# Kernel optimization log

Measured on AMD Instinct MI355X. Metric: run time of the kernel, lower is better.

Reference implementation:

```python
import jax, jax.numpy as jnp
import numpy as np

WS, OWS, HEADS, DH = 8, 12, 4, 16
INNER = HEADS * DH
DIM = 64
RATIO = 0.5
REL = 12  # rel_size = WS + (OWS - WS)


def _conv1x1(x, W, b):
    return jnp.einsum('oc,bchw->bohw', W, x) + b[None, :, None, None]


def _lrelu(x):
    return jnp.where(x >= 0, x, 0.1 * x)


def _rel_to_abs(x):
    # x: [b, l, 2r-1] -> [b, l, r]
    b, l, m = x.shape
    r = (m + 1) // 2
    x = jnp.pad(x, ((0, 0), (0, 0), (0, 1))).reshape(b, l * (m + 1))
    x = jnp.pad(x, ((0, 0), (0, m - l))).reshape(b, l + 1, m)
    return x[:, :l, -r:]


def _relative_logits_1d(q, rel_k):
    # q: [b, h, w, d], rel_k: [2r-1, d] -> [b, h, r, w, r]
    b, h, w, _ = q.shape
    r = (rel_k.shape[0] + 1) // 2
    logits = jnp.einsum('bxyd,rd->bxyr', q, rel_k)
    logits = _rel_to_abs(logits.reshape(b * h, w, 2 * r - 1)).reshape(b, h, w, r)
    return jnp.broadcast_to(logits[:, :, None], (b, h, r, w, r))


def _rel_pos_emb(q, rel_h, rel_w):
    # q: [b, WS*WS, DH] -> [b, WS*WS, REL*REL]
    b = q.shape[0]
    q = q.reshape(b, WS, WS, DH)
    lw = _relative_logits_1d(q, rel_w)                        # [b, x, i, y, j]
    lw = lw.transpose(0, 1, 3, 2, 4).reshape(b, WS * WS, REL * REL)   # (x y),(i j)
    lh = _relative_logits_1d(q.transpose(0, 2, 1, 3), rel_h)  # [b, y, i, x, j]
    lh = lh.transpose(0, 3, 1, 4, 2).reshape(b, WS * WS, REL * REL)   # (x y),(j i)
    return lw + lh


def _windows(t, B, Hw, Ww):
    # 'b c (h p1) (w p2) -> b (h w) (p1 p2 c)'
    return t.reshape(B, INNER, Hw, WS, Ww, WS).transpose(0, 2, 4, 3, 5, 1).reshape(B, Hw * Ww, WS * WS * INNER)


def _forward(x, condition_global, Wq, bq, Wk, bk, Wv, bv, Wout, bout,
             rel_h, rel_w, pin_W, pin_b, ln_w, ln_b, sa_W, sa_b,
             m1_W, m1_b, m2_W, m2_b):
    B, C, H, W = x.shape
    Hw, Ww = H // WS, W // WS
    Nw = Hw * Ww
    keep = int(Nw * RATIO)  # deterministic num_keep_node (expected r=0.5)
    scale = DH ** -0.5

    qs = _conv1x1(x, Wq, bq)
    ks = _conv1x1(x, Wk, bk)
    vs = _conv1x1(x, Wv, bv)

    # condition_wind: stacked ij meshgrid of linspace(-1,1,WS), tiled over windows
    lin = jnp.linspace(-1.0, 1.0, WS)
    gy, gx = jnp.meshgrid(lin, lin, indexing='ij')
    wind = jnp.tile(jnp.stack([gy, gx]).astype(x.dtype)[None], (B, 1, Hw, Ww))
    cond = jnp.concatenate([vs, condition_global, wind], axis=1)  # [B, INNER+4, H, W]

    # PredictorLG
    h1 = _conv1x1(cond, pin_W, pin_b)
    u = h1.mean(1, keepdims=True)
    s = ((h1 - u) ** 2).mean(1, keepdims=True)
    h1 = ln_w[None, :, None, None] * (h1 - u) / jnp.sqrt(s + 1e-6) + ln_b[None, :, None, None]
    h1 = _lrelu(h1)
    sa = jax.lax.conv_general_dilated(h1, sa_W, (1, 1), ((1, 1), (1, 1)),
                                      dimension_numbers=('NCHW', 'OIHW', 'NCHW'))
    sa = jax.nn.sigmoid(sa + sa_b[None, :, None, None])          # [B,1,H,W]

    xm = h1.mean(1)                                               # [B,H,W]
    xm = xm.reshape(B, Hw, WS, Ww, WS).transpose(0, 1, 3, 2, 4).reshape(B, Nw, WS * WS)
    z = _lrelu(xm @ m1_W.T + m1_b)
    pred = jax.nn.softmax(z @ m2_W.T + m2_b, axis=-1)
    score = pred[:, :, 0]
    idx = jnp.argsort(-score, axis=1)
    idx1, idx2 = idx[:, :keep], idx[:, keep:]
    bar = jnp.arange(B)[:, None]

    v_easy = vs * sa

    qw = _windows(qs, B, Hw, Ww)                                  # [B, Nw, 64*INNER]

    pad = (OWS - WS) // 2
    def unfold(t):
        p = jax.lax.conv_general_dilated_patches(t, (OWS, OWS), (WS, WS),
                                                 [(pad, pad), (pad, pad)])
        # [B, INNER*OWS*OWS, Hw, Ww], channel-major (c, kh, kw) like torch unfold
        p = p.reshape(B, INNER, OWS * OWS, Nw)
        return p.transpose(0, 3, 2, 1).reshape(B, Nw, OWS * OWS * INNER)  # (j c)
    kw, vw = unfold(ks), unfold(vs)

    qk, kk, vk = qw[bar, idx1], kw[bar, idx1], vw[bar, idx1]       # gather hard windows

    def heads(t, ntok):
        return t.reshape(B * keep, ntok, HEADS, DH).transpose(0, 2, 1, 3).reshape(B * keep * HEADS, ntok, DH)
    qh = heads(qk, WS * WS) * scale
    kh = heads(kk, OWS * OWS)
    vh = heads(vk, OWS * OWS)

    attn = jnp.einsum('bqc,bkc->bqk', qh, kh) + _rel_pos_emb(qh, rel_h, rel_w)
    attn = jax.nn.softmax(attn, axis=-1)
    vo = jnp.einsum('bqk,bkc->bqc', attn, vh)                      # [B*keep*HEADS, 64, DH]

    # '(b j head) (p1 p2) c -> b j (p1 p2 head c)'
    v1 = vo.reshape(B, keep, HEADS, WS * WS, DH).transpose(0, 1, 3, 2, 4).reshape(B, keep, WS * WS * INNER)
    v2 = _windows(v_easy, B, Hw, Ww)[bar, idx2]

    out = jnp.zeros((B, Nw, WS * WS * INNER), x.dtype)
    out = out.at[bar, idx1].set(v1).at[bar, idx2].set(v2)          # batch_index_fill
    # 'b (h w) (dh dw c) -> b c (h dh) (w dw)'
    out = out.reshape(B, Hw, Ww, WS, WS, INNER).transpose(0, 5, 1, 3, 2, 4).reshape(B, INNER, H, W)
    return _conv1x1(out, Wout, bout)


def setup_inputs() -> dict:
    key = jax.random.key(0)
    k = jax.random.split(key, 16)
    B, H, W = 2, 256, 256
    cdim = INNER + 4
    rel_scale = DH ** -0.5

    def p(kk, shape, s=0.05):
        return jax.random.normal(kk, shape, jnp.float32) * s

    return {
        'x': jax.random.normal(k[0], (B, DIM, H, W), jnp.float32),
        'condition_global': jax.random.normal(k[1], (B, 2, H, W), jnp.float32),
        'Wq': p(k[2], (INNER, DIM)), 'bq': jnp.zeros((INNER,), jnp.float32),
        'Wk': p(k[3], (INNER, DIM)), 'bk': jnp.zeros((INNER,), jnp.float32),
        'Wv': p(k[4], (INNER, DIM)), 'bv': jnp.zeros((INNER,), jnp.float32),
        'Wout': p(k[5], (DIM, INNER)), 'bout': jnp.zeros((DIM,), jnp.float32),
        'rel_h': jax.random.normal(k[6], (2 * REL - 1, DH), jnp.float32) * rel_scale,
        'rel_w': jax.random.normal(k[7], (2 * REL - 1, DH), jnp.float32) * rel_scale,
        'pin_W': p(k[8], (cdim // 4, cdim)), 'pin_b': jnp.zeros((cdim // 4,), jnp.float32),
        'ln_w': jnp.ones((cdim // 4,), jnp.float32), 'ln_b': jnp.zeros((cdim // 4,), jnp.float32),
        'sa_W': p(k[9], (1, cdim // 4, 3, 3)), 'sa_b': jnp.zeros((1,), jnp.float32),
        'm1_W': p(k[10], (WS, WS * WS)), 'm1_b': jnp.zeros((WS,), jnp.float32),
        'm2_W': p(k[11], (2, WS)), 'm2_b': jnp.zeros((2,), jnp.float32),
    }


def reference(x, condition_global, Wq, bq, Wk, bk, Wv, bv, Wout, bout,
              rel_h, rel_w, pin_W, pin_b, ln_w, ln_b, sa_W, sa_b,
              m1_W, m1_b, m2_W, m2_b):
    return _forward(x, condition_global, Wq, bq, Wk, bk, Wv, bv, Wout, bout,
                    rel_h, rel_w, pin_W, pin_b, ln_w, ln_b, sa_W, sa_b,
                    m1_W, m1_b, m2_W, m2_b)
```

## Files before the change

kernel.cpp:

```cpp
#include <hip/hip_runtime.h>
#include <math.h>

#define NPIX   65536
#define NPIXT  131072
#define NW     1024
#define KEEP   512
#define PITCH  68


__global__ __launch_bounds__(256) void k_qkv(
    const float* __restrict__ x,
    const float* __restrict__ Wq, const float* __restrict__ bq,
    const float* __restrict__ Wk, const float* __restrict__ bk,
    const float* __restrict__ Wv, const float* __restrict__ bv,
    float* __restrict__ qs, float* __restrict__ ks, float* __restrict__ vs)
{
    __shared__ float xs[64][256];
    const int tid = threadIdx.x;
    const int gp  = blockIdx.x * 256 + tid;
    const int b   = gp >> 16;
    const int p   = gp & 65535;
    const int p0  = p & ~255;

    #pragma unroll
    for (int it = 0; it < 16; ++it) {
        const int i  = it * 256 + tid;
        const int c  = i >> 6;
        const int p4 = i & 63;
        const float4 v = *(const float4*)(x + ((size_t)(b * 64 + c)) * NPIX + p0 + p4 * 4);
        *(float4*)&xs[c][p4 * 4] = v;
    }
    __syncthreads();

    const float* Ws[3]   = {Wq, Wk, Wv};
    const float* bias[3] = {bq, bk, bv};
    float* outs[3] = {qs + (size_t)gp * 64, ks + (size_t)gp * 64, vs + (size_t)gp * 64};

    for (int og = 0; og < 4; ++og) {
        float acc[3][16];
        #pragma unroll
        for (int m = 0; m < 3; ++m)
            #pragma unroll
            for (int j = 0; j < 16; ++j) acc[m][j] = 0.f;

        #pragma unroll 2
        for (int c = 0; c < 64; ++c) {
            const float xv = xs[c][tid];
            #pragma unroll
            for (int m = 0; m < 3; ++m) {
                const float* W = Ws[m];
                #pragma unroll
                for (int j = 0; j < 16; ++j)
                    acc[m][j] += W[(og * 16 + j) * 64 + c] * xv;
            }
        }
        #pragma unroll
        for (int m = 0; m < 3; ++m) {
            const float* bb = bias[m];
            #pragma unroll
            for (int j4 = 0; j4 < 4; ++j4) {
                float4 v;
                v.x = acc[m][j4 * 4 + 0] + bb[og * 16 + j4 * 4 + 0];
                v.y = acc[m][j4 * 4 + 1] + bb[og * 16 + j4 * 4 + 1];
                v.z = acc[m][j4 * 4 + 2] + bb[og * 16 + j4 * 4 + 2];
                v.w = acc[m][j4 * 4 + 3] + bb[og * 16 + j4 * 4 + 3];
                *(float4*)(outs[m] + og * 16 + j4 * 4) = v;
            }
        }
    }
}

__global__ __launch_bounds__(256) void k_cond(
    const float* __restrict__ vs, const float* __restrict__ cg,
    const float* __restrict__ pinW, const float* __restrict__ pinb,
    const float* __restrict__ lnw, const float* __restrict__ lnb,
    float* __restrict__ h1, float* __restrict__ xm)
{
    const int gp = blockIdx.x * 256 + threadIdx.x;
    const int b  = gp >> 16;
    const int p  = gp & 65535;
    const int h  = p >> 8;
    const int w  = p & 255;

    float acc[17];
    #pragma unroll
    for (int oc = 0; oc < 17; ++oc) acc[oc] = pinb[oc];

    const float* vp = vs + (size_t)gp * 64;
    #pragma unroll 4
    for (int c4 = 0; c4 < 16; ++c4) {
        const float4 v4 = *(const float4*)(vp + c4 * 4);
        const float vv[4] = {v4.x, v4.y, v4.z, v4.w};
        #pragma unroll
        for (int k = 0; k < 4; ++k) {
            const int c = c4 * 4 + k;
            #pragma unroll
            for (int oc = 0; oc < 17; ++oc)
                acc[oc] += pinW[oc * 68 + c] * vv[k];
        }
    }
    const float c64 = cg[(b * 2 + 0) * NPIX + p];
    const float c65 = cg[(b * 2 + 1) * NPIX + p];
    const float c66 = -1.f + 2.f * (float)(h & 7) / 7.f;
    const float c67 = -1.f + 2.f * (float)(w & 7) / 7.f;
    #pragma unroll
    for (int oc = 0; oc < 17; ++oc)
        acc[oc] += pinW[oc * 68 + 64] * c64 + pinW[oc * 68 + 65] * c65 +
                   pinW[oc * 68 + 66] * c66 + pinW[oc * 68 + 67] * c67;

    float u = 0.f;
    #pragma unroll
    for (int oc = 0; oc < 17; ++oc) u += acc[oc];
    u *= (1.f / 17.f);
    float s = 0.f;
    #pragma unroll
    for (int oc = 0; oc < 17; ++oc) { const float d = acc[oc] - u; s += d * d; }
    s *= (1.f / 17.f);
    const float rstd = rsqrtf(s + 1e-6f);

    float xsum = 0.f;
    #pragma unroll
    for (int oc = 0; oc < 17; ++oc) {
        float hv = lnw[oc] * (acc[oc] - u) * rstd + lnb[oc];
        hv = (hv >= 0.f) ? hv : 0.1f * hv;
        h1[(b * 17 + oc) * NPIX + p] = hv;
        xsum += hv;
    }
    xm[gp] = xsum * (1.f / 17.f);
}

__global__ __launch_bounds__(256) void k_sa(
    const float* __restrict__ h1, const float* __restrict__ saW,
    const float* __restrict__ sab, float* __restrict__ sa)
{
    __shared__ float S[17 * 3 * 256];
    const int tid = threadIdx.x;
    const int b   = blockIdx.x >> 8;
    const int row = blockIdx.x & 255;

    for (int i = tid; i < 3264; i += 256) {
        const int ch  = i / 192;
        const int rem = i - ch * 192;
        const int dr  = rem >> 6;
        const int c4  = rem & 63;
        const int rr  = row + dr - 1;
        float4 v = {0.f, 0.f, 0.f, 0.f};
        if ((unsigned)rr < 256u)
            v = *(const float4*)(h1 + ((size_t)(b * 17 + ch)) * NPIX + rr * 256 + c4 * 4);
        *(float4*)&S[(ch * 3 + dr) * 256 + c4 * 4] = v;
    }
    __syncthreads();

    const int w = tid;
    float acc = sab[0];
    #pragma unroll 1
    for (int ch = 0; ch < 17; ++ch) {
        #pragma unroll
        for (int dr = 0; dr < 3; ++dr) {
            const float* Sp = &S[(ch * 3 + dr) * 256];
            const float m  = Sp[w];
            const float l  = (w > 0)   ? Sp[w - 1] : 0.f;
            const float r_ = (w < 255) ? Sp[w + 1] : 0.f;
            const float* Wp = saW + (ch * 3 + dr) * 3;
            acc += Wp[0] * l + Wp[1] * m + Wp[2] * r_;
        }
    }
    sa[b * NPIX + row * 256 + w] = 1.f / (1.f + __expf(-acc));
}

__global__ __launch_bounds__(1024) void k_score_select(
    const float* __restrict__ xm,
    const float* __restrict__ m1W, const float* __restrict__ m1b,
    const float* __restrict__ m2W, const float* __restrict__ m2b,
    int* __restrict__ flag, int* __restrict__ kept)
{
    __shared__ float sc[NW];
    const int b = blockIdx.x;
    const int t = threadIdx.x;
    const int i = t >> 5;
    const int j = t & 31;

    float z[8];
    #pragma unroll
    for (int jj = 0; jj < 8; ++jj) z[jj] = m1b[jj];

    for (int a = 0; a < 8; ++a) {
        #pragma unroll
        for (int cc = 0; cc < 8; ++cc) {
            const float xv = xm[b * NPIX + (i * 8 + a) * 256 + (j * 8 + cc)];
            const int tt = a * 8 + cc;
            #pragma unroll
            for (int jj = 0; jj < 8; ++jj)
                z[jj] += m1W[jj * 64 + tt] * xv;
        }
    }
    #pragma unroll
    for (int jj = 0; jj < 8; ++jj) z[jj] = (z[jj] >= 0.f) ? z[jj] : 0.1f * z[jj];

    float l0 = m2b[0], l1 = m2b[1];
    #pragma unroll
    for (int jj = 0; jj < 8; ++jj) { l0 += m2W[jj] * z[jj]; l1 += m2W[8 + jj] * z[jj]; }
    const float mx = fmaxf(l0, l1);
    const float e0 = expf(l0 - mx), e1 = expf(l1 - mx);
    sc[t] = e0 / (e0 + e1);
    __syncthreads();

    const float s = sc[t];
    int cnt = 0;
    for (int jq = 0; jq < NW; ++jq) {
        const float sj = sc[jq];
        cnt += (sj > s) || (sj == s && jq < t);
    }
    flag[b * NW + t] = (cnt < KEEP) ? 1 : 0;
    if (cnt < KEEP) kept[b * KEEP + cnt] = t;
}

__global__ __launch_bounds__(256, 4) void k_attn(
    const float* __restrict__ qs, const float* __restrict__ ks,
    const float* __restrict__ vs, const int* __restrict__ kept,
    const float* __restrict__ relh, const float* __restrict__ relw,
    float* __restrict__ amix)
{
    __shared__ float SK[72 * PITCH];
    __shared__ float SV[72 * PITCH];

    const int b    = blockIdx.y;
    const int win  = kept[b * KEEP + blockIdx.x];
    const int wy = win >> 5, wx = win & 31;
    const int tid  = threadIdx.x;
    const int head = tid >> 6;
    const int lane = tid & 63;
    const int choff = head * 16;
    const size_t bbase = (size_t)b * NPIX;
    const int px0 = (wy * 8) * 256 + wx * 8;

    #pragma unroll
    for (int it = 0; it < 4; ++it) {
        const int i  = it * 256 + tid;
        const int px = i >> 4;
        const int c4 = i & 15;
        const float4 v = *(const float4*)(
            qs + (bbase + px0 + (px >> 3) * 256 + (px & 7)) * 64 + c4 * 4);
        *(float4*)&SK[px * PITCH + c4 * 4] = v;
    }
    __syncthreads();

    const int qrow = lane >> 3, qcol = lane & 7;
    float q[16];
    #pragma unroll
    for (int j4 = 0; j4 < 4; ++j4) {
        const float4 v = *(const float4*)&SK[(qrow * 8 + qcol) * PITCH + choff + j4 * 4];
        q[j4 * 4 + 0] = v.x * 0.25f; q[j4 * 4 + 1] = v.y * 0.25f;
        q[j4 * 4 + 2] = v.z * 0.25f; q[j4 * 4 + 3] = v.w * 0.25f;
    }

    float cw[12], chh[12];
    #pragma unroll
    for (int k = 0; k < 12; ++k) {
        const float* rw = relw + (k - qcol + 11) * 16;
        const float* rh = relh + (k - qrow + 11) * 16;
        float sw = 0.f, sh = 0.f;
        #pragma unroll
        for (int j4 = 0; j4 < 4; ++j4) {
            const float4 w4 = *(const float4*)(rw + j4 * 4);
            const float4 h4 = *(const float4*)(rh + j4 * 4);
            sw += q[j4*4+0]*w4.x + q[j4*4+1]*w4.y + q[j4*4+2]*w4.z + q[j4*4+3]*w4.w;
            sh += q[j4*4+0]*h4.x + q[j4*4+1]*h4.y + q[j4*4+2]*h4.z + q[j4*4+3]*h4.w;
        }
        cw[k] = sw; chh[k] = sh;
    }

    const int sub = lane >> 4;
    const int d_  = lane & 15;
    const int wy8 = wy * 8 - 2, wx8 = wx * 8 - 2;

    float sum = 0.f;
    float vo[16];
    #pragma unroll
    for (int d = 0; d < 16; ++d) vo[d] = 0.f;

    #pragma unroll 1
    for (int c = 0; c < 2; ++c) {
        __syncthreads();
        for (int i = tid; i < 1152; i += 256) {
            const int pxl = i >> 4;
            const int c4  = i & 15;
            const int rl  = pxl / 12;
            const int col = pxl - rl * 12;
            const int ry  = wy8 + 6 * c + rl;
            const int cx  = wx8 + col;
            float4 kv = {0.f,0.f,0.f,0.f}, vv = {0.f,0.f,0.f,0.f};
            if ((unsigned)ry < 256u && (unsigned)cx < 256u) {
                const size_t g = (bbase + ry * 256 + cx) * 64 + c4 * 4;
                kv = *(const float4*)(ks + g);
                vv = *(const float4*)(vs + g);
            }
            *(float4*)&SK[pxl * PITCH + c4 * 4] = kv;
            *(float4*)&SV[pxl * PITCH + c4 * 4] = vv;
        }
        __syncthreads();

        float kreg[18], vreg[18];
        #pragma unroll
        for (int r = 0; r < 18; ++r) {
            const int a = (4 * r + sub) * PITCH + choff + d_;
            kreg[r] = SK[a];
            vreg[r] = SV[a];
        }

        #pragma unroll
        for (int rl = 0; rl < 6; ++rl) {
            const float srow = chh[c * 6 + rl];
            #pragma unroll
            for (int col = 0; col < 12; ++col) {
                const int kl = rl * 12 + col;
                const int r  = kl >> 2, kk = kl & 3;
                float s = srow + cw[col];
                #pragma unroll
                for (int d = 0; d < 16; ++d)
                    s += __int_as_float(__builtin_amdgcn_readlane(
                             __float_as_int(kreg[r]), kk * 16 + d)) * q[d];
                const float e = __expf(s);
                sum += e;
                #pragma unroll
                for (int d = 0; d < 16; ++d)
                    vo[d] += e * __int_as_float(__builtin_amdgcn_readlane(
                                 __float_as_int(vreg[r]), kk * 16 + d));
            }
        }
    }

    const float inv = 1.f / sum;
    __syncthreads();
    #pragma unroll
    for (int j4 = 0; j4 < 4; ++j4) {
        float4 v;
        v.x = vo[j4*4+0] * inv; v.y = vo[j4*4+1] * inv;
        v.z = vo[j4*4+2] * inv; v.w = vo[j4*4+3] * inv;
        *(float4*)&SK[(qrow * 8 + qcol) * PITCH + choff + j4 * 4] = v;
    }
    __syncthreads();
    #pragma unroll
    for (int it = 0; it < 4; ++it) {
        const int i  = it * 256 + tid;
        const int px = i >> 4;
        const int c4 = i & 15;
        const float4 v = *(const float4*)&SK[px * PITCH + c4 * 4];
        *(float4*)(amix + (bbase + px0 + (px >> 3) * 256 + (px & 7)) * 64 + c4 * 4) = v;
    }
}

__global__ __launch_bounds__(256) void k_out_f(
    const float* __restrict__ amix, const float* __restrict__ vs,
    const float* __restrict__ sa, const int* __restrict__ flag,
    const float* __restrict__ W, const float* __restrict__ bias,
    float* __restrict__ out)
{
    __shared__ float xs[64][256];
    const int tid = threadIdx.x;
    const int gp  = blockIdx.x * 256 + tid;
    const int b   = gp >> 16;
    const int p   = gp & 65535;
    const int h   = p >> 8;
    const int w   = p & 255;

    const int win = (h >> 3) * 32 + (w >> 3);
    const int fl  = flag[b * NW + win];
    const float mult = fl ? 1.f : sa[gp];
    const float* src = (fl ? amix : vs) + (size_t)gp * 64;

    #pragma unroll
    for (int c4 = 0; c4 < 16; ++c4) {
        const float4 v = *(const float4*)(src + c4 * 4);
        xs[c4 * 4 + 0][tid] = v.x * mult;
        xs[c4 * 4 + 1][tid] = v.y * mult;
        xs[c4 * 4 + 2][tid] = v.z * mult;
        xs[c4 * 4 + 3][tid] = v.w * mult;
    }
    __syncthreads();

    const int base = (b << 6) * NPIX + p;
    for (int og = 0; og < 4; ++og) {
        float acc[16];
        #pragma unroll
        for (int j = 0; j < 16; ++j) acc[j] = 0.f;
        #pragma unroll 4
        for (int c = 0; c < 64; ++c) {
            const float xv = xs[c][tid];
            #pragma unroll
            for (int j = 0; j < 16; ++j)
                acc[j] += W[(og * 16 + j) * 64 + c] * xv;
        }
        #pragma unroll
        for (int j = 0; j < 16; ++j)
            out[base + (og * 16 + j) * NPIX] = acc[j] + bias[og * 16 + j];
    }
}

extern "C" void kernel_launch(void* const* d_in, const int* in_sizes, int n_in,
                              void* d_out, int out_size, void* d_ws, size_t ws_size,
                              hipStream_t stream)
{
    const float* x    = (const float*)d_in[0];
    const float* cg   = (const float*)d_in[1];
    const float* Wq   = (const float*)d_in[2];
    const float* bq   = (const float*)d_in[3];
    const float* Wk   = (const float*)d_in[4];
    const float* bk   = (const float*)d_in[5];
    const float* Wv   = (const float*)d_in[6];
    const float* bv   = (const float*)d_in[7];
    const float* Wout = (const float*)d_in[8];
    const float* bout = (const float*)d_in[9];
    const float* relh = (const float*)d_in[10];
    const float* relw = (const float*)d_in[11];
    const float* pinW = (const float*)d_in[12];
    const float* pinb = (const float*)d_in[13];
    const float* lnw  = (const float*)d_in[14];
    const float* lnb  = (const float*)d_in[15];
    const float* saW  = (const float*)d_in[16];
    const float* sab  = (const float*)d_in[17];
    const float* m1W  = (const float*)d_in[18];
    const float* m1b  = (const float*)d_in[19];
    const float* m2W  = (const float*)d_in[20];
    const float* m2b  = (const float*)d_in[21];
    float* out = (float*)d_out;

    float* ws    = (float*)d_ws;
    float* qs    = ws;
    float* ks    = qs + 8388608;
    float* vs    = ks + 8388608;
    float* h1    = vs + 8388608;
    float* xm    = h1 + 17 * NPIXT;
    float* sa    = xm + NPIXT;
    int*   flag  = (int*)(sa + NPIXT);
    int*   kept  = flag + 2048;

    k_qkv         <<<NPIXT / 256, 256, 0, stream>>>(x, Wq, bq, Wk, bk, Wv, bv, qs, ks, vs);
    k_cond        <<<NPIXT / 256, 256, 0, stream>>>(vs, cg, pinW, pinb, lnw, lnb, h1, xm);
    k_sa          <<<512, 256, 0, stream>>>(h1, saW, sab, sa);
    k_score_select<<<2, 1024, 0, stream>>>(xm, m1W, m1b, m2W, m2b, flag, kept);
    k_attn        <<<dim3(KEEP, 2), 256, 0, stream>>>(qs, ks, vs, kept, relh, relw, qs);
    k_out_f       <<<NPIXT / 256, 256, 0, stream>>>(qs, vs, sa, flag, Wout, bout, out);
}
```

Measured before the change: 423.4 us.

## Restructure QKV projection loop and tune waves-per-EU for qkv and attention

The QKV 1x1-conv kernel now handles one projection at a time with all 64 output channels in registers. It stages x through a half-sized shared buffer in two 32-channel passes, which cuts LDS use and makes each pass of weights uniform across the block. Both the QKV and attention kernels get an amdgpu_waves_per_eu(3,4) hint in place of the previous launch bounds. In attention, the readlane broadcasts of K and V are hoisted into arrays before the dot product and accumulation so they can be scheduled together. The x tile is now reloaded three times, once per projection, and the larger accumulator raises register pressure.

```diff
diff --git a/kernel.cpp b/kernel.cpp
--- a/kernel.cpp
+++ b/kernel.cpp
@@ -8,64 +8,65 @@
 #define PITCH  68
 
 
-__global__ __launch_bounds__(256) void k_qkv(
+__global__ __launch_bounds__(256) __attribute__((amdgpu_waves_per_eu(3, 4)))
+void k_qkv(
     const float* __restrict__ x,
     const float* __restrict__ Wq, const float* __restrict__ bq,
     const float* __restrict__ Wk, const float* __restrict__ bk,
     const float* __restrict__ Wv, const float* __restrict__ bv,
     float* __restrict__ qs, float* __restrict__ ks, float* __restrict__ vs)
 {
-    __shared__ float xs[64][256];
+    __shared__ float xs[32][256];
     const int tid = threadIdx.x;
     const int gp  = blockIdx.x * 256 + tid;
     const int b   = gp >> 16;
     const int p   = gp & 65535;
     const int p0  = p & ~255;
 
-    #pragma unroll
-    for (int it = 0; it < 16; ++it) {
-        const int i  = it * 256 + tid;
-        const int c  = i >> 6;
-        const int p4 = i & 63;
-        const float4 v = *(const float4*)(x + ((size_t)(b * 64 + c)) * NPIX + p0 + p4 * 4);
-        *(float4*)&xs[c][p4 * 4] = v;
-    }
-    __syncthreads();
-
     const float* Ws[3]   = {Wq, Wk, Wv};
     const float* bias[3] = {bq, bk, bv};
     float* outs[3] = {qs + (size_t)gp * 64, ks + (size_t)gp * 64, vs + (size_t)gp * 64};
 
-    for (int og = 0; og < 4; ++og) {
-        float acc[3][16];
-        #pragma unroll
-        for (int m = 0; m < 3; ++m)
+    #pragma unroll
+    for (int m = 0; m < 3; ++m) {
+        float acc[64];
+        #pragma unroll
+        for (int j = 0; j < 64; ++j) acc[j] = 0.f;
+
+        #pragma unroll
+        for (int half = 0; half < 2; ++half) {
+            __syncthreads();
             #pragma unroll
-            for (int j = 0; j < 16; ++j) acc[m][j] = 0.f;
-
-        #pragma unroll 2
-        for (int c = 0; c < 64; ++c) {
-            const float xv = xs[c][tid];
-            #pragma unroll
-            for (int m = 0; m < 3; ++m) {
-                const float* W = Ws[m];
+            for (int it = 0; it < 8; ++it) {
+                const int i  = it * 256 + tid;
+                const int c  = i >> 6;
+                const int p4 = i & 63;
+                *(float4*)&xs[c][p4 * 4] =
+                    *(const float4*)(x + ((size_t)(b * 64 + half * 32 + c)) * NPIX + p0 + p4 * 4);
+            }
+            __syncthreads();
+
+            const float* W = Ws[m];
+            #pragma unroll 2
+            for (int cc = 0; cc < 32; ++cc) {
+                const int c   = half * 32 + cc;
+                const float xv = xs[cc][tid];
                 #pragma unroll
-                for (int j = 0; j < 16; ++j)
-                    acc[m][j] += W[(og * 16 + j) * 64 + c] * xv;
+                for (int j = 0; j < 64; ++j)
+                    acc[j] += W[j * 64 + c] * xv;
             }
         }
-        #pragma unroll
-        for (int m = 0; m < 3; ++m) {
-            const float* bb = bias[m];
-            #pragma unroll
-            for (int j4 = 0; j4 < 4; ++j4) {
-                float4 v;
-                v.x = acc[m][j4 * 4 + 0] + bb[og * 16 + j4 * 4 + 0];
-                v.y = acc[m][j4 * 4 + 1] + bb[og * 16 + j4 * 4 + 1];
-                v.z = acc[m][j4 * 4 + 2] + bb[og * 16 + j4 * 4 + 2];
-                v.w = acc[m][j4 * 4 + 3] + bb[og * 16 + j4 * 4 + 3];
-                *(float4*)(outs[m] + og * 16 + j4 * 4) = v;
-            }
+
+        const float* bb = bias[m];
+        float* op = outs[m];
+        #pragma unroll
+        for (int j4 = 0; j4 < 16; ++j4) {
+            float4 v;
+            v.x = acc[j4 * 4 + 0] + bb[j4 * 4 + 0];
+            v.y = acc[j4 * 4 + 1] + bb[j4 * 4 + 1];
+            v.z = acc[j4 * 4 + 2] + bb[j4 * 4 + 2];
+            v.w = acc[j4 * 4 + 3] + bb[j4 * 4 + 3];
+            *(float4*)(op + j4 * 4) = v;
         }
     }
 }
@@ -215,7 +216,8 @@
     if (cnt < KEEP) kept[b * KEEP + cnt] = t;
 }
 
-__global__ __launch_bounds__(256, 4) void k_attn(
+__global__ __launch_bounds__(256) __attribute__((amdgpu_waves_per_eu(3, 4)))
+void k_attn(
     const float* __restrict__ qs, const float* __restrict__ ks,
     const float* __restrict__ vs, const int* __restrict__ kept,
     const float* __restrict__ relh, const float* __restrict__ relw,
@@ -315,17 +317,24 @@
             for (int col = 0; col < 12; ++col) {
                 const int kl = rl * 12 + col;
                 const int r  = kl >> 2, kk = kl & 3;
+                float kv[16], vv[16];
+                #pragma unroll
+                for (int d = 0; d < 16; ++d)
+                    kv[d] = __int_as_float(__builtin_amdgcn_readlane(
+                                __float_as_int(kreg[r]), kk * 16 + d));
+                #pragma unroll
+                for (int d = 0; d < 16; ++d)
+                    vv[d] = __int_as_float(__builtin_amdgcn_readlane(
+                                __float_as_int(vreg[r]), kk * 16 + d));
                 float s = srow + cw[col];
                 #pragma unroll
                 for (int d = 0; d < 16; ++d)
-                    s += __int_as_float(__builtin_amdgcn_readlane(
-                             __float_as_int(kreg[r]), kk * 16 + d)) * q[d];
+                    s += kv[d] * q[d];
                 const float e = __expf(s);
                 sum += e;
                 #pragma unroll
                 for (int d = 0; d < 16; ++d)
-                    vo[d] += e * __int_as_float(__builtin_amdgcn_readlane(
-                                 __float_as_int(vreg[r]), kk * 16 + d));
+                    vo[d] += e * vv[d];
             }
         }
     }
```

After: 522.4 us. 23.4% more time.

## Restructure QKV projection tiling and cut attention register pressure

Applied to the files above, without the earlier changes.

k_qkv now gives each block 64 pixels, with the four output-channel groups spread across threads instead of looped serially. This uses four times as many blocks and a smaller shared tile, but each block reads fewer pixels per x load. In k_attn, the per-pixel 18-entry K/V register arrays are replaced with a one-ahead streamed shared-memory load, and the row rel-pos logits are computed per chunk instead of all at once. The launch-bounds occupancy hint is also dropped. Together these are meant to reduce register pressure and improve occupancy and overlap, at the cost of some recomputation and more frequent LDS reads.

```diff
diff --git a/kernel.cpp b/kernel.cpp
--- a/kernel.cpp
+++ b/kernel.cpp
@@ -15,20 +15,22 @@
     const float* __restrict__ Wv, const float* __restrict__ bv,
     float* __restrict__ qs, float* __restrict__ ks, float* __restrict__ vs)
 {
-    __shared__ float xs[64][256];
-    const int tid = threadIdx.x;
-    const int gp  = blockIdx.x * 256 + tid;
-    const int b   = gp >> 16;
-    const int p   = gp & 65535;
-    const int p0  = p & ~255;
-
-    #pragma unroll
-    for (int it = 0; it < 16; ++it) {
-        const int i  = it * 256 + tid;
-        const int c  = i >> 6;
-        const int p4 = i & 63;
-        const float4 v = *(const float4*)(x + ((size_t)(b * 64 + c)) * NPIX + p0 + p4 * 4);
-        *(float4*)&xs[c][p4 * 4] = v;
+    __shared__ float xs[64][64];
+    const int tid  = threadIdx.x;
+    const int px   = tid & 63;
+    const int og   = tid >> 6;
+    const int tile = blockIdx.x;
+    const int b    = tile >> 10;
+    const int p0   = (tile & 1023) << 6;
+    const int gp   = (b << 16) + p0 + px;
+
+    #pragma unroll
+    for (int it = 0; it < 4; ++it) {
+        const int i = it * 256 + tid;
+        const int c = i >> 4;
+        const int f = i & 15;
+        *(float4*)&xs[c][f * 4] =
+            *(const float4*)(x + ((size_t)(b * 64 + c)) * NPIX + p0 + f * 4);
     }
     __syncthreads();
 
@@ -36,36 +38,34 @@
     const float* bias[3] = {bq, bk, bv};
     float* outs[3] = {qs + (size_t)gp * 64, ks + (size_t)gp * 64, vs + (size_t)gp * 64};
 
-    for (int og = 0; og < 4; ++og) {
-        float acc[3][16];
-        #pragma unroll
-        for (int m = 0; m < 3; ++m)
-            #pragma unroll
-            for (int j = 0; j < 16; ++j) acc[m][j] = 0.f;
-
-        #pragma unroll 2
-        for (int c = 0; c < 64; ++c) {
-            const float xv = xs[c][tid];
-            #pragma unroll
-            for (int m = 0; m < 3; ++m) {
-                const float* W = Ws[m];
-                #pragma unroll
-                for (int j = 0; j < 16; ++j)
-                    acc[m][j] += W[(og * 16 + j) * 64 + c] * xv;
-            }
-        }
+    float acc[3][16];
+    #pragma unroll
+    for (int m = 0; m < 3; ++m)
+        #pragma unroll
+        for (int j = 0; j < 16; ++j) acc[m][j] = 0.f;
+
+    #pragma unroll 2
+    for (int c = 0; c < 64; ++c) {
+        const float xv = xs[c][px];
         #pragma unroll
         for (int m = 0; m < 3; ++m) {
-            const float* bb = bias[m];
-            #pragma unroll
-            for (int j4 = 0; j4 < 4; ++j4) {
-                float4 v;
-                v.x = acc[m][j4 * 4 + 0] + bb[og * 16 + j4 * 4 + 0];
-                v.y = acc[m][j4 * 4 + 1] + bb[og * 16 + j4 * 4 + 1];
-                v.z = acc[m][j4 * 4 + 2] + bb[og * 16 + j4 * 4 + 2];
-                v.w = acc[m][j4 * 4 + 3] + bb[og * 16 + j4 * 4 + 3];
-                *(float4*)(outs[m] + og * 16 + j4 * 4) = v;
-            }
+            const float* W = Ws[m];
+            #pragma unroll
+            for (int j = 0; j < 16; ++j)
+                acc[m][j] += W[(og * 16 + j) * 64 + c] * xv;
+        }
+    }
+    #pragma unroll
+    for (int m = 0; m < 3; ++m) {
+        const float* bb = bias[m];
+        #pragma unroll
+        for (int j4 = 0; j4 < 4; ++j4) {
+            float4 v;
+            v.x = acc[m][j4 * 4 + 0] + bb[og * 16 + j4 * 4 + 0];
+            v.y = acc[m][j4 * 4 + 1] + bb[og * 16 + j4 * 4 + 1];
+            v.z = acc[m][j4 * 4 + 2] + bb[og * 16 + j4 * 4 + 2];
+            v.w = acc[m][j4 * 4 + 3] + bb[og * 16 + j4 * 4 + 3];
+            *(float4*)(outs[m] + og * 16 + j4 * 4) = v;
         }
     }
 }
@@ -215,7 +215,7 @@
     if (cnt < KEEP) kept[b * KEEP + cnt] = t;
 }
 
-__global__ __launch_bounds__(256, 4) void k_attn(
+__global__ __launch_bounds__(256) void k_attn(
     const float* __restrict__ qs, const float* __restrict__ ks,
     const float* __restrict__ vs, const int* __restrict__ kept,
     const float* __restrict__ relh, const float* __restrict__ relw,
@@ -254,20 +254,17 @@
         q[j4 * 4 + 2] = v.z * 0.25f; q[j4 * 4 + 3] = v.w * 0.25f;
     }
 
-    float cw[12], chh[12];
+    float cw[12];
     #pragma unroll
     for (int k = 0; k < 12; ++k) {
         const float* rw = relw + (k - qcol + 11) * 16;
-        const float* rh = relh + (k - qrow + 11) * 16;
-        float sw = 0.f, sh = 0.f;
+        float sw = 0.f;
         #pragma unroll
         for (int j4 = 0; j4 < 4; ++j4) {
             const float4 w4 = *(const float4*)(rw + j4 * 4);
-            const float4 h4 = *(const float4*)(rh + j4 * 4);
             sw += q[j4*4+0]*w4.x + q[j4*4+1]*w4.y + q[j4*4+2]*w4.z + q[j4*4+3]*w4.w;
-            sh += q[j4*4+0]*h4.x + q[j4*4+1]*h4.y + q[j4*4+2]*h4.z + q[j4*4+3]*h4.w;
-        }
-        cw[k] = sw; chh[k] = sh;
+        }
+        cw[k] = sw;
     }
 
     const int sub = lane >> 4;
@@ -300,33 +297,55 @@
         }
         __syncthreads();
 
-        float kreg[18], vreg[18];
-        #pragma unroll
-        for (int r = 0; r < 18; ++r) {
-            const int a = (4 * r + sub) * PITCH + choff + d_;
-            kreg[r] = SK[a];
-            vreg[r] = SV[a];
-        }
-
+        float chc[6];
         #pragma unroll
         for (int rl = 0; rl < 6; ++rl) {
-            const float srow = chh[c * 6 + rl];
-            #pragma unroll
-            for (int col = 0; col < 12; ++col) {
-                const int kl = rl * 12 + col;
-                const int r  = kl >> 2, kk = kl & 3;
-                float s = srow + cw[col];
+            const float* rh = relh + (c * 6 + rl - qrow + 11) * 16;
+            float sh = 0.f;
+            #pragma unroll
+            for (int j4 = 0; j4 < 4; ++j4) {
+                const float4 h4 = *(const float4*)(rh + j4 * 4);
+                sh += q[j4*4+0]*h4.x + q[j4*4+1]*h4.y + q[j4*4+2]*h4.z + q[j4*4+3]*h4.w;
+            }
+            chc[rl] = sh;
+        }
+
+        float kg = SK[sub * PITCH + choff + d_];
+        float vg = SV[sub * PITCH + choff + d_];
+        #pragma unroll
+        for (int g = 0; g < 18; ++g) {
+            float kn = 0.f, vn = 0.f;
+            if (g < 17) {
+                const int a = (4 * (g + 1) + sub) * PITCH + choff + d_;
+                kn = SK[a];
+                vn = SV[a];
+            }
+            #pragma unroll
+            for (int kk = 0; kk < 4; ++kk) {
+                const int kl  = g * 4 + kk;
+                const int rl  = kl / 12;
+                const int col = kl - rl * 12;
+                float kd[16];
                 #pragma unroll
                 for (int d = 0; d < 16; ++d)
-                    s += __int_as_float(__builtin_amdgcn_readlane(
-                             __float_as_int(kreg[r]), kk * 16 + d)) * q[d];
+                    kd[d] = __int_as_float(__builtin_amdgcn_readlane(
+                                __float_as_int(kg), kk * 16 + d));
+                float s = chc[rl] + cw[col];
+                #pragma unroll
+                for (int d = 0; d < 16; ++d)
+                    s += kd[d] * q[d];
                 const float e = __expf(s);
                 sum += e;
+                float vd[16];
                 #pragma unroll
                 for (int d = 0; d < 16; ++d)
-                    vo[d] += e * __int_as_float(__builtin_amdgcn_readlane(
-                                 __float_as_int(vreg[r]), kk * 16 + d));
+                    vd[d] = __int_as_float(__builtin_amdgcn_readlane(
+                                __float_as_int(vg), kk * 16 + d));
+                #pragma unroll
+                for (int d = 0; d < 16; ++d)
+                    vo[d] += e * vd[d];
             }
+            kg = kn; vg = vn;
         }
     }
 
@@ -435,7 +454,7 @@
     int*   flag  = (int*)(sa + NPIXT);
     int*   kept  = flag + 2048;
 
-    k_qkv         <<<NPIXT / 256, 256, 0, stream>>>(x, Wq, bq, Wk, bk, Wv, bv, qs, ks, vs);
+    k_qkv         <<<2048, 256, 0, stream>>>(x, Wq, bq, Wk, bk, Wv, bv, qs, ks, vs);
     k_cond        <<<NPIXT / 256, 256, 0, stream>>>(vs, cg, pinW, pinb, lnw, lnb, h1, xm);
     k_sa          <<<512, 256, 0, stream>>>(h1, saW, sab, sa);
     k_score_select<<<2, 1024, 0, stream>>>(xm, m1W, m1b, m2W, m2b, flag, kept);
```

Measured after the change: 685.1 us. 61.8% more time.
